# Performance work log

Hardware: AMD Instinct MI355X
Metric: run time of the kernel (lower is better)

The kernel has to match this reference:

```python
import jax, jax.numpy as jnp
import numpy as np


def _conv1x1(t, W, b):
    # 1x1 conv == per-pixel channel GEMM: [B,C,H,W] x [O,C] -> [B,O,H,W]
    return jnp.einsum('bchw,oc->bohw', t, W) + b[None, :, None, None]


def setup_inputs() -> dict:
    key = jax.random.key(0)
    ks = jax.random.split(key, 10)
    B, C, H, W = 8, 256, 96, 96
    s = 1.0 / np.sqrt(C)
    inp = {
        'x': jax.random.normal(ks[0], (B, C, H, W), dtype=jnp.float32),
        'Wq': jax.random.normal(ks[1], (C, C), dtype=jnp.float32) * s,
        'bq': jax.random.normal(ks[2], (C,), dtype=jnp.float32) * 0.01,
        'Wk': jax.random.normal(ks[3], (C, C), dtype=jnp.float32) * s,
        'bk': jax.random.normal(ks[4], (C,), dtype=jnp.float32) * 0.01,
        'Wv': jax.random.normal(ks[5], (C, C), dtype=jnp.float32) * s,
        'bv': jax.random.normal(ks[6], (C,), dtype=jnp.float32) * 0.01,
        'Ws': jax.random.normal(ks[7], (C, C), dtype=jnp.float32) * s,
        'bs': jax.random.normal(ks[8], (C,), dtype=jnp.float32) * 0.01,
        # torch init is zeros; use a nonzero scalar so the attention branch matters
        'gamma': jax.random.normal(ks[9], (1,), dtype=jnp.float32) * 0.5,
    }
    return inp


def reference(x, Wq, bq, Wk, bk, Wv, bv, Ws, bs, gamma):
    B, C, H, W = x.shape
    N = H * W
    # query: [B, N, C]
    q = _conv1x1(x, Wq, bq).reshape(B, C, N).transpose(0, 2, 1)
    # key: 1x1 conv, then stride-3 1x1 conv (== subsample every 3rd pixel, then GEMM)
    k = _conv1x1(x, Wk, bk)
    k = _conv1x1(k[:, :, ::3, ::3], Ws, bs)
    Ns = k.shape[2] * k.shape[3]
    k = k.reshape(B, C, Ns)
    energy = jnp.einsum('bnc,bcm->bnm', q, k)       # [B, N, Ns]
    attn = jax.nn.softmax(energy, axis=-1)
    # value: same 1x1 conv + strided 1x1 conv pipeline
    v = _conv1x1(x, Wv, bv)
    v = _conv1x1(v[:, :, ::3, ::3], Ws, bs).reshape(B, C, Ns)
    out = jnp.einsum('bcm,bnm->bcn', v, attn).reshape(B, C, H, W)
    return gamma[0] * out + x
```

## Files before the change

kernel.cpp:

```cpp
#include <hip/hip_runtime.h>

typedef _Float16 f16;
typedef _Float16 f16x8 __attribute__((ext_vector_type(8)));
typedef __fp16 fp16x2 __attribute__((ext_vector_type(2)));
typedef float f32x4 __attribute__((ext_vector_type(4)));

#define CDIM 256
#define NPIX 9216
#define NB 8

__device__ __forceinline__ f32x4 mfma16(f16x8 a, f16x8 b, f32x4 c) {
  return __builtin_amdgcn_mfma_f32_16x16x32_f16(a, b, c, 0, 0, 0);
}
__device__ __forceinline__ f16x8 ld8(const f16* p) { return *(const f16x8*)p; }

__device__ __forceinline__ void stage16(const void* g, void* l) {
  __builtin_amdgcn_global_load_lds((const __attribute__((address_space(1))) unsigned int*)g,
                                   (__attribute__((address_space(3))) unsigned int*)l, 16, 0, 0);
}
#define S_BARRIER() do { asm volatile("" ::: "memory"); __builtin_amdgcn_s_barrier(); asm volatile("" ::: "memory"); } while (0)
#define WAIT_VM(N) do { asm volatile("s_waitcnt vmcnt(" #N ")" ::: "memory"); __builtin_amdgcn_sched_barrier(0); } while (0)

__device__ __forceinline__ unsigned pkrtz(float a, float b) {
  union { fp16x2 h; unsigned u; } cv;
  cv.h = __builtin_amdgcn_cvt_pkrtz(a, b);
  return cv.u;
}
union U8 { f16x8 v; unsigned u[4]; };
__device__ __forceinline__ f16x8 mk8(unsigned a, unsigned b, unsigned c, unsigned d) {
  U8 r; r.u[0] = a; r.u[1] = b; r.u[2] = c; r.u[3] = d; return r.v;
}


__global__ void prep_weights(const float* __restrict__ Wq,
                             const float* __restrict__ Wk, const float* __restrict__ bk,
                             const float* __restrict__ Wv, const float* __restrict__ bv,
                             const float* __restrict__ Ws, const float* __restrict__ bs,
                             f16* __restrict__ WqF, f16* __restrict__ Wk2H, f16* __restrict__ Wv2H,
                             float* __restrict__ bk2, float* __restrict__ bv2) {
  int o = blockIdx.x, c = threadIdx.x;
  float ak = 0.f, av = 0.f;
  for (int i = 0; i < CDIM; ++i) {
    float w = Ws[o*CDIM + i];
    ak += w * Wk[i*CDIM + c];
    av += w * Wv[i*CDIM + c];
  }
  Wk2H[o*CDIM + c] = (f16)ak;
  Wv2H[o*CDIM + c] = (f16)av;
  {
    int og = o >> 4, sp = c >> 5;
    int lane = 16*((c >> 3) & 3) + (o & 15);
    size_t byte = (size_t)(og*8 + sp)*1024 + (size_t)lane*16 + (c & 7)*2;
    *(f16*)((char*)WqF + byte) = (f16)Wq[o*CDIM + c];
  }
  if (c == 0) {
    float sk = 0.f, sv = 0.f;
    for (int i = 0; i < CDIM; ++i) { float w = Ws[o*CDIM + i]; sk += w*bk[i]; sv += w*bv[i]; }
    bk2[o] = sk + bs[o];
    bv2[o] = sv + bs[o];
  }
}

__global__ void transpose_x(const float* __restrict__ x, char* __restrict__ xT) {
  __shared__ f16 tile[32][34];
  int c0 = blockIdx.x * 32, n0 = blockIdx.y * 32, b = blockIdx.z;
  int tx = threadIdx.x, ty = threadIdx.y;
#pragma unroll
  for (int j = 0; j < 4; ++j) {
    int cl = ty + 8*j;
    tile[cl][tx] = (f16)x[(size_t)(b*CDIM + c0 + cl)*NPIX + n0 + tx];
  }
  __syncthreads();
  int tid = ty*32 + tx;
  if (tid < 128) {
    int nl = tid >> 2, u = tid & 3;
    int n = n0 + nl;
    int cu = (c0 >> 3) + u;
    f16x8 v;
#pragma unroll
    for (int e = 0; e < 8; ++e) v[e] = tile[8*u + e][nl];
    size_t byte = (size_t)(b*NPIX + n)*512 + (size_t)((cu ^ (n & 7)) << 4);
    *(f16x8*)(xT + byte) = v;
  }
}

__global__ __launch_bounds__(256) void compute_kv(
    const char* __restrict__ xT, const f16* __restrict__ Wk2H, const f16* __restrict__ Wv2H,
    const float* __restrict__ bk2, const float* __restrict__ bv2,
    char* __restrict__ kB, char* __restrict__ vB) {
  int ch = blockIdx.x;
  int m0 = ch * 32;
  int b = blockIdx.y;
  int tid = threadIdx.x;
  int w = tid >> 6, lane = tid & 63, l15 = lane & 15, q = lane >> 4;
  size_t chbase = (size_t)(b*32 + ch)*16384;

  const char* xrow[2]; int xn7[2];
#pragma unroll
  for (int mt2 = 0; mt2 < 2; ++mt2) {
    int m = m0 + 16*mt2 + l15;
    int n = 288*(m >> 5) + 3*(m & 31);
    xrow[mt2] = xT + (size_t)(b*NPIX + n)*512;
    xn7[mt2] = n & 7;
  }
  const f16 *kwb[4], *vwb[4];
#pragma unroll
  for (int t = 0; t < 4; ++t) {
    kwb[t] = Wk2H + (size_t)(64*w + 16*t + l15)*CDIM + 8*q;
    vwb[t] = Wv2H + (size_t)(64*w + 16*t + l15)*CDIM + 8*q;
  }
  f32x4 accK[2][4] = {};
  f32x4 accV[4][2] = {};
  for (int ks = 0; ks < 8; ++ks) {
    f16x8 am[2], wk[4], wv[4];
#pragma unroll
    for (int mt2 = 0; mt2 < 2; ++mt2)
      am[mt2] = *(const f16x8*)(xrow[mt2] + (((q + 4*ks) ^ xn7[mt2]) << 4));
#pragma unroll
    for (int t = 0; t < 4; ++t) { wk[t] = ld8(kwb[t] + 32*ks); wv[t] = ld8(vwb[t] + 32*ks); }
#pragma unroll
    for (int mt2 = 0; mt2 < 2; ++mt2)
#pragma unroll
      for (int ot = 0; ot < 4; ++ot) {
        accK[mt2][ot] = mfma16(am[mt2], wk[ot], accK[mt2][ot]);
        accV[ot][mt2] = mfma16(wv[ot], am[mt2], accV[ot][mt2]);
      }
  }
#pragma unroll
  for (int mt2 = 0; mt2 < 2; ++mt2)
#pragma unroll
    for (int ot = 0; ot < 4; ++ot) {
      int cin = 64*w + 16*ot + l15;
      float bo = bk2[cin];
      int f = 2*(cin >> 5) + mt2;
      int q_s = (cin >> 2) & 3;
      int e_s = 4*((cin >> 4) & 1) + (cin & 3);
      size_t fb = chbase + (size_t)f*1024 + (size_t)(16*q_s)*16 + e_s*2;
#pragma unroll
      for (int r = 0; r < 4; ++r) {
        int krel15 = 4*q + r;
        *(f16*)(kB + fb + (size_t)krel15*16) = (f16)(accK[mt2][ot][r] + bo);
      }
    }
#pragma unroll
  for (int ct = 0; ct < 4; ++ct) {
    f32x4 bv4 = *(const f32x4*)(bv2 + 64*w + 16*ct + 4*q);
#pragma unroll
    for (int mt2 = 0; mt2 < 2; ++mt2) {
      int q_s = (l15 >> 2) & 3;
      int e_s = 4*mt2 + (l15 & 3);
#pragma unroll
      for (int r = 0; r < 4; ++r) {
        int c = 64*w + 16*ct + 4*q + r;
        size_t byte = chbase + (size_t)(c >> 4)*1024
                    + (size_t)(16*q_s + (c & 15))*16 + e_s*2;
        *(f16*)(vB + byte) = (f16)(accV[ct][mt2][r] + bv4[r]);
      }
    }
  }
}

__global__ __launch_bounds__(256, 2) void attention(
    const char* __restrict__ xT, const f16* __restrict__ WqF, const float* __restrict__ bq,
    const char* __restrict__ kB, const char* __restrict__ vB,
    const float* __restrict__ xg, const float* __restrict__ gamma_p,
    float* __restrict__ out) {
  __shared__ char lds[65536];

  int bid = blockIdx.x;
  int b = bid & 7;
  int tile = bid >> 3;
  int tid = threadIdx.x;
  int w = tid >> 6, lane = tid & 63, l15 = lane & 15, q = lane >> 4;
  int n0w = tile*64 + w*16;
  int lane16 = lane * 16;

  const char* kBb = kB + (size_t)b*524288;
  const char* vBb = vB + (size_t)b*524288;

  {
    int so = tid * 16;
#pragma unroll
    for (int r = 0; r < 4; ++r) stage16(kBb + so + r*4096, lds + so + r*4096);
#pragma unroll
    for (int r = 0; r < 4; ++r) stage16(vBb + so + r*4096, lds + 16384 + so + r*4096);
  }

  f16x8 qf[8];
  {
    f16x8 xb[8];
    int n = n0w + l15;
    const char* xrow = xT + (size_t)(b*NPIX + n)*512;
    int n7 = n & 7;
#pragma unroll
    for (int sp = 0; sp < 8; ++sp)
      xb[sp] = *(const f16x8*)(xrow + (((4*sp + q) ^ n7) << 4));
    f32x4 qacc[16];
#pragma unroll
    for (int og = 0; og < 16; ++og) {
      f32x4 acc = {0.f, 0.f, 0.f, 0.f};
#pragma unroll
      for (int sp = 0; sp < 8; ++sp) {
        f16x8 wa = *(const f16x8*)((const char*)WqF + (size_t)(og*8 + sp)*1024 + lane16);
        acc = mfma16(wa, xb[sp], acc);
      }
      f32x4 bq4 = *(const f32x4*)(bq + og*16 + 4*q);
#pragma unroll
      for (int r = 0; r < 4; ++r) acc[r] += bq4[r];
      qacc[og] = acc;
    }
#pragma unroll
    for (int s = 0; s < 8; ++s)
      qf[s] = mk8(pkrtz(qacc[2*s][0],   qacc[2*s][1]),
                  pkrtz(qacc[2*s][2],   qacc[2*s][3]),
                  pkrtz(qacc[2*s+1][0], qacc[2*s+1][1]),
                  pkrtz(qacc[2*s+1][2], qacc[2*s+1][3]));
  }

  f32x4 O[16];
#pragma unroll
  for (int i = 0; i < 16; ++i) O[i] = (f32x4){0.f, 0.f, 0.f, 0.f};
  float m_run = -3e38f, l_run = 0.f;

  for (int t = 0; t < 32; ++t) {
    char* curb = lds + ((t & 1) << 15);
    if (t < 31) {
      const char* ksrc = kBb + (size_t)(t + 1)*16384;
      const char* vsrc = vBb + (size_t)(t + 1)*16384;
      char* kd = lds + (((t + 1) & 1) << 15);
      int so = tid * 16;
#pragma unroll
      for (int r = 0; r < 4; ++r) stage16(ksrc + so + r*4096, kd + so + r*4096);
#pragma unroll
      for (int r = 0; r < 4; ++r) stage16(vsrc + so + r*4096, kd + 16384 + so + r*4096);
      WAIT_VM(8);
    } else {
      WAIT_VM(0);
    }
    S_BARRIER();

    f32x4 S0 = {0.f, 0.f, 0.f, 0.f}, S1 = {0.f, 0.f, 0.f, 0.f};
    __builtin_amdgcn_s_setprio(1);
#pragma unroll
    for (int s = 0; s < 8; ++s) {
      f16x8 kf0 = *(const f16x8*)(curb + (2*s)*1024 + lane16);
      S0 = mfma16(kf0, qf[s], S0);
      f16x8 kf1 = *(const f16x8*)(curb + (2*s + 1)*1024 + lane16);
      S1 = mfma16(kf1, qf[s], S1);
    }
    __builtin_amdgcn_s_setprio(0);

    float mx = fmaxf(fmaxf(fmaxf(S0[0], S0[1]), fmaxf(S0[2], S0[3])),
                     fmaxf(fmaxf(S1[0], S1[1]), fmaxf(S1[2], S1[3])));
    mx = fmaxf(mx, __shfl_xor(mx, 16));
    mx = fmaxf(mx, __shfl_xor(mx, 32));
    if (!__all(mx <= m_run + 8.0f)) {
      float mn = fmaxf(m_run, mx);
      float al = __expf(m_run - mn);
      m_run = mn;
      l_run *= al;
#pragma unroll
      for (int i = 0; i < 16; ++i)
#pragma unroll
        for (int r = 0; r < 4; ++r) O[i][r] *= al;
    }
    float ls = 0.f;
#pragma unroll
    for (int r = 0; r < 4; ++r) { S0[r] = __expf(S0[r] - m_run); ls += S0[r]; }
#pragma unroll
    for (int r = 0; r < 4; ++r) { S1[r] = __expf(S1[r] - m_run); ls += S1[r]; }
    l_run += ls;

    f16x8 pf = mk8(pkrtz(S0[0], S0[1]), pkrtz(S0[2], S0[3]),
                   pkrtz(S1[0], S1[1]), pkrtz(S1[2], S1[3]));

    __builtin_amdgcn_s_setprio(1);
#pragma unroll
    for (int cg = 0; cg < 16; ++cg) {
      f16x8 vf = *(const f16x8*)(curb + 16384 + cg*1024 + lane16);
      O[cg] = mfma16(vf, pf, O[cg]);
    }
    __builtin_amdgcn_s_setprio(0);
    S_BARRIER();
  }

  l_run += __shfl_xor(l_run, 16);
  l_run += __shfl_xor(l_run, 32);
  float inv = 1.0f / l_run;
  float g = gamma_p[0];
  int n = n0w + l15;
#pragma unroll
  for (int cg = 0; cg < 16; ++cg)
#pragma unroll
    for (int r = 0; r < 4; ++r) {
      int c = 16*cg + 4*q + r;
      size_t idx = (size_t)(b*CDIM + c)*NPIX + n;
      out[idx] = g * (O[cg][r] * inv) + xg[idx];
    }
}

extern "C" void kernel_launch(void* const* d_in, const int* in_sizes, int n_in,
                              void* d_out, int out_size, void* d_ws, size_t ws_size,
                              hipStream_t stream) {
  (void)in_sizes; (void)n_in; (void)out_size; (void)ws_size;
  const float* x     = (const float*)d_in[0];
  const float* Wq    = (const float*)d_in[1];
  const float* bq    = (const float*)d_in[2];
  const float* Wk    = (const float*)d_in[3];
  const float* bk    = (const float*)d_in[4];
  const float* Wv    = (const float*)d_in[5];
  const float* bv    = (const float*)d_in[6];
  const float* Ws    = (const float*)d_in[7];
  const float* bs    = (const float*)d_in[8];
  const float* gamma = (const float*)d_in[9];

  char* ws = (char*)d_ws;
  float* bk2 = (float*)(ws);
  float* bv2 = (float*)(ws + 1024);
  char* xT   = ws + 4096;
  char* kB   = ws + 4096 + 37748736;
  char* vB   = kB + 4194304;
  f16* WqF   = (f16*)(vB + 4194304);
  f16* Wk2H  = WqF + 65536;
  f16* Wv2H  = Wk2H + 65536;

  prep_weights<<<256, 256, 0, stream>>>(Wq, Wk, bk, Wv, bv, Ws, bs, WqF, Wk2H, Wv2H, bk2, bv2);
  transpose_x<<<dim3(8, 288, 8), dim3(32, 8), 0, stream>>>(x, xT);
  compute_kv<<<dim3(32, 8), 256, 0, stream>>>(xT, Wk2H, Wv2H, bk2, bv2, kB, vB);
  attention<<<1152, 256, 0, stream>>>(xT, WqF, bq, kB, vB, x, gamma, (float*)d_out);
}
```

Before: 206.3 us.

## Process two query row groups per wave to reuse K/V fragments, pre-swizzle Wk/Wv

The attention kernel now has each wave handle 32 query pixels as two 16-row groups with separate online-softmax state. Each K and V fragment read from LDS feeds two MFMAs, which halves K/V staging traffic per query and halves the grid to 576 blocks. The fused K/V weights are also written in the MFMA fragment layout, so compute_kv loads them with one contiguous 16-byte load per lane instead of strided row loads. The cost is roughly doubled accumulator register pressure, which may reduce occupancy, and fewer blocks to fill the GPU.

```diff
diff --git a/kernel.cpp b/kernel.cpp
--- a/kernel.cpp
+++ b/kernel.cpp
@@ -36,7 +36,7 @@
                              const float* __restrict__ Wk, const float* __restrict__ bk,
                              const float* __restrict__ Wv, const float* __restrict__ bv,
                              const float* __restrict__ Ws, const float* __restrict__ bs,
-                             f16* __restrict__ WqF, f16* __restrict__ Wk2H, f16* __restrict__ Wv2H,
+                             f16* __restrict__ WqF, f16* __restrict__ WkF, f16* __restrict__ WvF,
                              float* __restrict__ bk2, float* __restrict__ bv2) {
   int o = blockIdx.x, c = threadIdx.x;
   float ak = 0.f, av = 0.f;
@@ -45,13 +45,12 @@
     ak += w * Wk[i*CDIM + c];
     av += w * Wv[i*CDIM + c];
   }
-  Wk2H[o*CDIM + c] = (f16)ak;
-  Wv2H[o*CDIM + c] = (f16)av;
   {
-    int og = o >> 4, sp = c >> 5;
-    int lane = 16*((c >> 3) & 3) + (o & 15);
-    size_t byte = (size_t)(og*8 + sp)*1024 + (size_t)lane*16 + (c & 7)*2;
-    *(f16*)((char*)WqF + byte) = (f16)Wq[o*CDIM + c];
+    size_t fbyte = (size_t)((o >> 4)*8 + (c >> 5))*1024
+                 + (size_t)(16*((c >> 3) & 3) + (o & 15))*16 + (c & 7)*2;
+    *(f16*)((char*)WqF + fbyte) = (f16)Wq[o*CDIM + c];
+    *(f16*)((char*)WkF + fbyte) = (f16)ak;
+    *(f16*)((char*)WvF + fbyte) = (f16)av;
   }
   if (c == 0) {
     float sk = 0.f, sv = 0.f;
@@ -85,7 +84,7 @@
 }
 
 __global__ __launch_bounds__(256) void compute_kv(
-    const char* __restrict__ xT, const f16* __restrict__ Wk2H, const f16* __restrict__ Wv2H,
+    const char* __restrict__ xT, const f16* __restrict__ WkF, const f16* __restrict__ WvF,
     const float* __restrict__ bk2, const float* __restrict__ bv2,
     char* __restrict__ kB, char* __restrict__ vB) {
   int ch = blockIdx.x;
@@ -103,12 +102,9 @@
     xrow[mt2] = xT + (size_t)(b*NPIX + n)*512;
     xn7[mt2] = n & 7;
   }
-  const f16 *kwb[4], *vwb[4];
-#pragma unroll
-  for (int t = 0; t < 4; ++t) {
-    kwb[t] = Wk2H + (size_t)(64*w + 16*t + l15)*CDIM + 8*q;
-    vwb[t] = Wv2H + (size_t)(64*w + 16*t + l15)*CDIM + 8*q;
-  }
+  const char* wkf = (const char*)WkF + (size_t)lane*16;
+  const char* wvf = (const char*)WvF + (size_t)lane*16;
+
   f32x4 accK[2][4] = {};
   f32x4 accV[4][2] = {};
   for (int ks = 0; ks < 8; ++ks) {
@@ -117,7 +113,10 @@
     for (int mt2 = 0; mt2 < 2; ++mt2)
       am[mt2] = *(const f16x8*)(xrow[mt2] + (((q + 4*ks) ^ xn7[mt2]) << 4));
 #pragma unroll
-    for (int t = 0; t < 4; ++t) { wk[t] = ld8(kwb[t] + 32*ks); wv[t] = ld8(vwb[t] + 32*ks); }
+    for (int t = 0; t < 4; ++t) {
+      wk[t] = *(const f16x8*)(wkf + (size_t)((4*w + t)*8 + ks)*1024);
+      wv[t] = *(const f16x8*)(wvf + (size_t)((4*w + t)*8 + ks)*1024);
+    }
 #pragma unroll
     for (int mt2 = 0; mt2 < 2; ++mt2)
 #pragma unroll
@@ -172,7 +171,7 @@
   int tile = bid >> 3;
   int tid = threadIdx.x;
   int w = tid >> 6, lane = tid & 63, l15 = lane & 15, q = lane >> 4;
-  int n0w = tile*64 + w*16;
+  int n0w = tile*128 + w*32;
   int lane16 = lane * 16;
 
   const char* kBb = kB + (size_t)b*524288;
@@ -186,10 +185,11 @@
     for (int r = 0; r < 4; ++r) stage16(vBb + so + r*4096, lds + 16384 + so + r*4096);
   }
 
-  f16x8 qf[8];
-  {
+  f16x8 qf[2][8];
+#pragma unroll
+  for (int g = 0; g < 2; ++g) {
     f16x8 xb[8];
-    int n = n0w + l15;
+    int n = n0w + 16*g + l15;
     const char* xrow = xT + (size_t)(b*NPIX + n)*512;
     int n7 = n & 7;
 #pragma unroll
@@ -211,16 +211,20 @@
     }
 #pragma unroll
     for (int s = 0; s < 8; ++s)
-      qf[s] = mk8(pkrtz(qacc[2*s][0],   qacc[2*s][1]),
-                  pkrtz(qacc[2*s][2],   qacc[2*s][3]),
-                  pkrtz(qacc[2*s+1][0], qacc[2*s+1][1]),
-                  pkrtz(qacc[2*s+1][2], qacc[2*s+1][3]));
-  }
-
-  f32x4 O[16];
-#pragma unroll
-  for (int i = 0; i < 16; ++i) O[i] = (f32x4){0.f, 0.f, 0.f, 0.f};
-  float m_run = -3e38f, l_run = 0.f;
+      qf[g][s] = mk8(pkrtz(qacc[2*s][0],   qacc[2*s][1]),
+                     pkrtz(qacc[2*s][2],   qacc[2*s][3]),
+                     pkrtz(qacc[2*s+1][0], qacc[2*s+1][1]),
+                     pkrtz(qacc[2*s+1][2], qacc[2*s+1][3]));
+  }
+
+  f32x4 OA[16], OB[16];
+#pragma unroll
+  for (int i = 0; i < 16; ++i) {
+    OA[i] = (f32x4){0.f, 0.f, 0.f, 0.f};
+    OB[i] = (f32x4){0.f, 0.f, 0.f, 0.f};
+  }
+  float mA = -3e38f, lA = 0.f;
+  float mB = -3e38f, lB = 0.f;
 
   for (int t = 0; t < 32; ++t) {
     char* curb = lds + ((t & 1) << 15);
@@ -239,63 +243,92 @@
     }
     S_BARRIER();
 
-    f32x4 S0 = {0.f, 0.f, 0.f, 0.f}, S1 = {0.f, 0.f, 0.f, 0.f};
+    f32x4 SA0 = {0.f,0.f,0.f,0.f}, SA1 = {0.f,0.f,0.f,0.f};
+    f32x4 SB0 = {0.f,0.f,0.f,0.f}, SB1 = {0.f,0.f,0.f,0.f};
     __builtin_amdgcn_s_setprio(1);
 #pragma unroll
     for (int s = 0; s < 8; ++s) {
       f16x8 kf0 = *(const f16x8*)(curb + (2*s)*1024 + lane16);
-      S0 = mfma16(kf0, qf[s], S0);
+      SA0 = mfma16(kf0, qf[0][s], SA0);
+      SB0 = mfma16(kf0, qf[1][s], SB0);
       f16x8 kf1 = *(const f16x8*)(curb + (2*s + 1)*1024 + lane16);
-      S1 = mfma16(kf1, qf[s], S1);
+      SA1 = mfma16(kf1, qf[0][s], SA1);
+      SB1 = mfma16(kf1, qf[1][s], SB1);
     }
     __builtin_amdgcn_s_setprio(0);
 
-    float mx = fmaxf(fmaxf(fmaxf(S0[0], S0[1]), fmaxf(S0[2], S0[3])),
-                     fmaxf(fmaxf(S1[0], S1[1]), fmaxf(S1[2], S1[3])));
-    mx = fmaxf(mx, __shfl_xor(mx, 16));
-    mx = fmaxf(mx, __shfl_xor(mx, 32));
-    if (!__all(mx <= m_run + 8.0f)) {
-      float mn = fmaxf(m_run, mx);
-      float al = __expf(m_run - mn);
-      m_run = mn;
-      l_run *= al;
+    float mxA = fmaxf(fmaxf(fmaxf(SA0[0], SA0[1]), fmaxf(SA0[2], SA0[3])),
+                      fmaxf(fmaxf(SA1[0], SA1[1]), fmaxf(SA1[2], SA1[3])));
+    mxA = fmaxf(mxA, __shfl_xor(mxA, 16));
+    mxA = fmaxf(mxA, __shfl_xor(mxA, 32));
+    if (!__all(mxA <= mA + 8.0f)) {
+      float mn = fmaxf(mA, mxA);
+      float al = __expf(mA - mn);
+      mA = mn;
+      lA *= al;
 #pragma unroll
       for (int i = 0; i < 16; ++i)
 #pragma unroll
-        for (int r = 0; r < 4; ++r) O[i][r] *= al;
-    }
-    float ls = 0.f;
-#pragma unroll
-    for (int r = 0; r < 4; ++r) { S0[r] = __expf(S0[r] - m_run); ls += S0[r]; }
-#pragma unroll
-    for (int r = 0; r < 4; ++r) { S1[r] = __expf(S1[r] - m_run); ls += S1[r]; }
-    l_run += ls;
-
-    f16x8 pf = mk8(pkrtz(S0[0], S0[1]), pkrtz(S0[2], S0[3]),
-                   pkrtz(S1[0], S1[1]), pkrtz(S1[2], S1[3]));
+        for (int r = 0; r < 4; ++r) OA[i][r] *= al;
+    }
+    float lsA = 0.f;
+#pragma unroll
+    for (int r = 0; r < 4; ++r) { SA0[r] = __expf(SA0[r] - mA); lsA += SA0[r]; }
+#pragma unroll
+    for (int r = 0; r < 4; ++r) { SA1[r] = __expf(SA1[r] - mA); lsA += SA1[r]; }
+    lA += lsA;
+    f16x8 pfA = mk8(pkrtz(SA0[0], SA0[1]), pkrtz(SA0[2], SA0[3]),
+                    pkrtz(SA1[0], SA1[1]), pkrtz(SA1[2], SA1[3]));
+
+    float mxB = fmaxf(fmaxf(fmaxf(SB0[0], SB0[1]), fmaxf(SB0[2], SB0[3])),
+                      fmaxf(fmaxf(SB1[0], SB1[1]), fmaxf(SB1[2], SB1[3])));
+    mxB = fmaxf(mxB, __shfl_xor(mxB, 16));
+    mxB = fmaxf(mxB, __shfl_xor(mxB, 32));
+    if (!__all(mxB <= mB + 8.0f)) {
+      float mn = fmaxf(mB, mxB);
+      float al = __expf(mB - mn);
+      mB = mn;
+      lB *= al;
+#pragma unroll
+      for (int i = 0; i < 16; ++i)
+#pragma unroll
+        for (int r = 0; r < 4; ++r) OB[i][r] *= al;
+    }
+    float lsB = 0.f;
+#pragma unroll
+    for (int r = 0; r < 4; ++r) { SB0[r] = __expf(SB0[r] - mB); lsB += SB0[r]; }
+#pragma unroll
+    for (int r = 0; r < 4; ++r) { SB1[r] = __expf(SB1[r] - mB); lsB += SB1[r]; }
+    lB += lsB;
+    f16x8 pfB = mk8(pkrtz(SB0[0], SB0[1]), pkrtz(SB0[2], SB0[3]),
+                    pkrtz(SB1[0], SB1[1]), pkrtz(SB1[2], SB1[3]));
 
     __builtin_amdgcn_s_setprio(1);
 #pragma unroll
     for (int cg = 0; cg < 16; ++cg) {
       f16x8 vf = *(const f16x8*)(curb + 16384 + cg*1024 + lane16);
-      O[cg] = mfma16(vf, pf, O[cg]);
+      OA[cg] = mfma16(vf, pfA, OA[cg]);
+      OB[cg] = mfma16(vf, pfB, OB[cg]);
     }
     __builtin_amdgcn_s_setprio(0);
     S_BARRIER();
   }
 
-  l_run += __shfl_xor(l_run, 16);
-  l_run += __shfl_xor(l_run, 32);
-  float inv = 1.0f / l_run;
   float g = gamma_p[0];
-  int n = n0w + l15;
+  lA += __shfl_xor(lA, 16);
+  lA += __shfl_xor(lA, 32);
+  lB += __shfl_xor(lB, 16);
+  lB += __shfl_xor(lB, 32);
+  float invA = 1.0f / lA, invB = 1.0f / lB;
+  int nA = n0w + l15, nB = n0w + 16 + l15;
 #pragma unroll
   for (int cg = 0; cg < 16; ++cg)
 #pragma unroll
     for (int r = 0; r < 4; ++r) {
       int c = 16*cg + 4*q + r;
-      size_t idx = (size_t)(b*CDIM + c)*NPIX + n;
-      out[idx] = g * (O[cg][r] * inv) + xg[idx];
+      size_t rowbase = (size_t)(b*CDIM + c)*NPIX;
+      out[rowbase + nA] = g * (OA[cg][r] * invA) + xg[rowbase + nA];
+      out[rowbase + nB] = g * (OB[cg][r] * invB) + xg[rowbase + nB];
     }
 }
 
@@ -321,11 +354,11 @@
   char* kB   = ws + 4096 + 37748736;
   char* vB   = kB + 4194304;
   f16* WqF   = (f16*)(vB + 4194304);
-  f16* Wk2H  = WqF + 65536;
-  f16* Wv2H  = Wk2H + 65536;
-
-  prep_weights<<<256, 256, 0, stream>>>(Wq, Wk, bk, Wv, bv, Ws, bs, WqF, Wk2H, Wv2H, bk2, bv2);
+  f16* WkF   = WqF + 65536;
+  f16* WvF   = WkF + 65536;
+
+  prep_weights<<<256, 256, 0, stream>>>(Wq, Wk, bk, Wv, bv, Ws, bs, WqF, WkF, WvF, bk2, bv2);
   transpose_x<<<dim3(8, 288, 8), dim3(32, 8), 0, stream>>>(x, xT);
-  compute_kv<<<dim3(32, 8), 256, 0, stream>>>(xT, Wk2H, Wv2H, bk2, bv2, kB, vB);
-  attention<<<1152, 256, 0, stream>>>(xT, WqF, bq, kB, vB, x, gamma, (float*)d_out);
-}
+  compute_kv<<<dim3(32, 8), 256, 0, stream>>>(xT, WkF, WvF, bk2, bv2, kB, vB);
+  attention<<<576, 256, 0, stream>>>(xT, WqF, bq, kB, vB, x, gamma, (float*)d_out);
+}
```

After: 335.9 us. 1.63x slower.
